# Kernel optimization log

Hardware: AMD Instinct MI355X
Metric: run time of the kernel (lower is better)

## Reference

```python
import jax, jax.numpy as jnp
import numpy as np
import math

NEG = -1000000.0


def setup_inputs() -> dict:
    key = jax.random.key(0)
    ks = jax.random.split(key, 8)
    B, S, D = 4, 2048, 1024
    std = 1.0 / math.sqrt(D)
    return {
        "queries": jax.random.normal(ks[0], (B, S, D), jnp.float32),
        "keys": jax.random.normal(ks[1], (B, S, D), jnp.float32),
        "values": jax.random.normal(ks[2], (B, S, D), jnp.float32),
        "valid_len": jax.random.randint(ks[3], (B,), 1, S, dtype=jnp.int64 if jax.config.jax_enable_x64 else jnp.int32),
        "W_q": jax.random.normal(ks[4], (D, D), jnp.float32) * std,
        "W_k": jax.random.normal(ks[5], (D, D), jnp.float32) * std,
        "W_v": jax.random.normal(ks[6], (D, D), jnp.float32) * std,
        "W_o": jax.random.normal(ks[7], (D, D), jnp.float32) * std,
    }


def reference(queries, keys, values, valid_len, W_q, W_k, W_v, W_o):
    NUM_HEADS = 16
    B, S, D = queries.shape
    hd = D // NUM_HEADS

    def split_heads(x):
        # (B, S, D) -> (B, H, S, hd)
        return x.reshape(B, -1, NUM_HEADS, hd).transpose(0, 2, 1, 3)

    # nn.Linear with weight W applies x @ W.T
    q = split_heads(queries @ W_q.T)
    k = split_heads(keys @ W_k.T)
    v = split_heads(values @ W_v.T)

    scale = 1.0 / math.sqrt(hd)
    scores = jnp.einsum('bhqd,bhkd->bhqk', q, k) * scale  # (B, H, Sq, Sk)

    # key-padding mask from valid_len: positions >= valid_len are masked
    kpos = jnp.arange(scores.shape[-1])
    pad_mask = kpos[None, None, None, :] >= valid_len[:, None, None, None]
    scores = jnp.where(pad_mask, NEG, scores)
    attn = jax.nn.softmax(scores, axis=-1)

    out = jnp.einsum('bhqk,bhkd->bhqd', attn, v)  # (B, H, Sq, hd)
    out = out.transpose(0, 2, 1, 3).reshape(B, -1, D)
    return out @ W_o.T
```

## Files before the change

kernel.cpp:

```cpp
#include <hip/hip_runtime.h>
#include <hip/hip_bf16.h>

using bf16_t = __bf16;
using bf16x8 = __attribute__((ext_vector_type(8))) __bf16;
using bf16x4 = __attribute__((ext_vector_type(4))) __bf16;
using bf16x2 = __attribute__((ext_vector_type(2))) __bf16;
using f32x4  = __attribute__((ext_vector_type(4))) float;

#define S_  2048
#define D_  1024

typedef __attribute__((address_space(1))) unsigned int glb_u32;
typedef __attribute__((address_space(3))) unsigned int lds_u32;

__device__ __forceinline__ void async_cp16(const void* g, void* lds) {
    __builtin_amdgcn_global_load_lds(
        (glb_u32*)(unsigned long long)g,
        (lds_u32*)(unsigned int)(unsigned long long)lds,
        16, 0, 0);
}

__global__ __launch_bounds__(256) void cast_f32_bf16(const float* __restrict__ s,
                                                     bf16_t* __restrict__ d, int n4) {
    int i = blockIdx.x * 256 + threadIdx.x;
    if (i >= n4) return;
    float4 f = reinterpret_cast<const float4*>(s)[i];
    bf16x4 o;
    o[0] = (bf16_t)f.x; o[1] = (bf16_t)f.y; o[2] = (bf16_t)f.z; o[3] = (bf16_t)f.w;
    reinterpret_cast<bf16x4*>(d)[i] = o;
}

__global__ __launch_bounds__(256) void cast2_f32_bf16(const float* __restrict__ a, const float* __restrict__ b,
                                                      bf16_t* __restrict__ oa, bf16_t* __restrict__ ob, int n4) {
    int i = blockIdx.x * 256 + threadIdx.x;
    if (i >= n4) return;
    const float* s = blockIdx.y ? b : a;
    bf16_t*      d = blockIdx.y ? ob : oa;
    float4 f = reinterpret_cast<const float4*>(s)[i];
    bf16x4 o;
    o[0] = (bf16_t)f.x; o[1] = (bf16_t)f.y; o[2] = (bf16_t)f.z; o[3] = (bf16_t)f.w;
    reinterpret_cast<bf16x4*>(d)[i] = o;
}

__global__ __launch_bounds__(256) void cast4_f32_bf16(const float* __restrict__ a, const float* __restrict__ b,
                                                      const float* __restrict__ c, const float* __restrict__ dd,
                                                      bf16_t* __restrict__ oa, bf16_t* __restrict__ ob,
                                                      bf16_t* __restrict__ oc, bf16_t* __restrict__ od, int n4) {
    int i = blockIdx.x * 256 + threadIdx.x;
    if (i >= n4) return;
    const float* s; bf16_t* d;
    int w = blockIdx.y;
    if      (w == 0) { s = a;  d = oa; }
    else if (w == 1) { s = b;  d = ob; }
    else if (w == 2) { s = c;  d = oc; }
    else             { s = dd; d = od; }
    float4 f = reinterpret_cast<const float4*>(s)[i];
    bf16x4 o;
    o[0] = (bf16_t)f.x; o[1] = (bf16_t)f.y; o[2] = (bf16_t)f.z; o[3] = (bf16_t)f.w;
    reinterpret_cast<bf16x4*>(d)[i] = o;
}

template <int OUTMODE>
__global__ __launch_bounds__(256) void gemm_bt(const bf16_t* __restrict__ A,
                                               const bf16_t* __restrict__ Bt,
                                               void* __restrict__ Cv, float scale) {
    __shared__ bf16_t As[2][128 * 32];
    __shared__ bf16_t Bs[2][128 * 32];
    const int K = 1024;
    int tid  = threadIdx.x;
    int lane = tid & 63;
    int w    = tid >> 6;
    int l15  = lane & 15, quad = lane >> 4;

    int bid = blockIdx.y * gridDim.x + blockIdx.x;
    int xcd = bid & 7, idx = bid >> 3;
    int m0 = (xcd * 8 + (idx & 7)) * 128;
    int n0 = (idx >> 3) * 128;
    int wm = (w >> 1) * 64, wn = (w & 1) * 64;

    const bf16_t* Ag = A  + (size_t)(m0 + (tid >> 2)) * K + (tid & 3) * 8;
    const bf16_t* Bg = Bt + (size_t)(n0 + (tid >> 2)) * K + (tid & 3) * 8;

    f32x4 acc[4][4] = {};

    async_cp16(Ag,                  &As[0][tid * 8]);
    async_cp16(Ag + (size_t)64 * K, &As[0][tid * 8 + 2048]);
    async_cp16(Bg,                  &Bs[0][tid * 8]);
    async_cp16(Bg + (size_t)64 * K, &Bs[0][tid * 8 + 2048]);
    __syncthreads();

    for (int k0 = 0; k0 < K; k0 += 32) {
        int cur = (k0 >> 5) & 1;
        if (k0 + 32 < K) {
            int nxt = cur ^ 1;
            async_cp16(Ag + k0 + 32,                  &As[nxt][tid * 8]);
            async_cp16(Ag + k0 + 32 + (size_t)64 * K, &As[nxt][tid * 8 + 2048]);
            async_cp16(Bg + k0 + 32,                  &Bs[nxt][tid * 8]);
            async_cp16(Bg + k0 + 32 + (size_t)64 * K, &Bs[nxt][tid * 8 + 2048]);
        }
        bf16x8 af[4], bfr[4];
#pragma unroll
        for (int t = 0; t < 4; t++) {
            af[t]  = *reinterpret_cast<const bf16x8*>(&As[cur][(wm + t * 16 + l15) * 32 + quad * 8]);
            bfr[t] = *reinterpret_cast<const bf16x8*>(&Bs[cur][(wn + t * 16 + l15) * 32 + quad * 8]);
        }
#pragma unroll
        for (int mt = 0; mt < 4; mt++)
#pragma unroll
            for (int nt = 0; nt < 4; nt++)
                acc[mt][nt] = __builtin_amdgcn_mfma_f32_16x16x32_bf16(af[mt], bfr[nt], acc[mt][nt], 0, 0, 0);
        __syncthreads();
    }

#pragma unroll
    for (int mt = 0; mt < 4; mt++)
#pragma unroll
        for (int nt = 0; nt < 4; nt++) {
            if (OUTMODE == 2) {
                int m = m0 + wm + mt * 16 + quad * 4;
                int n = n0 + wn + nt * 16 + l15;
                bf16x4 o4;
#pragma unroll
                for (int r = 0; r < 4; r++) o4[r] = (bf16_t)(acc[mt][nt][r] * scale);
                size_t vrow = (size_t)((m >> 11) * 16 + (n >> 6)) * 64 + (n & 63);
                int ml = m & 2047;
                int mp = (ml & ~31) | (((ml >> 2) & 3) << 3) | (((ml >> 4) & 1) << 2);
                *reinterpret_cast<bf16x4*>(&((bf16_t*)Cv)[vrow * S_ + mp]) = o4;
            } else {
#pragma unroll
                for (int r = 0; r < 4; r++) {
                    int m = m0 + wm + mt * 16 + quad * 4 + r;
                    int n = n0 + wn + nt * 16 + l15;
                    size_t idx2 = (size_t)m * 1024 + n;
                    if (OUTMODE == 1) reinterpret_cast<float*>(Cv)[idx2] = acc[mt][nt][r] * scale;
                    else              reinterpret_cast<bf16_t*>(Cv)[idx2] = (bf16_t)(acc[mt][nt][r] * scale);
                }
            }
        }
}

__global__ __launch_bounds__(256) void attn_fused(const bf16_t* __restrict__ Qp,
                                                  const bf16_t* __restrict__ Kp,
                                                  const bf16_t* __restrict__ Vt,
                                                  const int* __restrict__ vlen_p,
                                                  bf16_t* __restrict__ Out) {
    __shared__ bf16_t smem[4][64 * 64];

    int tid  = threadIdx.x;
    int lane = tid & 63, w = tid >> 6;
    int l15  = lane & 15, quad = lane >> 4;

    int nk[4], ord[4] = {0, 1, 2, 3};
#pragma unroll
    for (int i = 0; i < 4; i++) nk[i] = (vlen_p[i] + 63) >> 6;
#pragma unroll
    for (int i = 0; i < 3; i++)
#pragma unroll
        for (int j = 0; j < 3 - i; j++)
            if (nk[ord[j + 1]] > nk[ord[j]]) { int t = ord[j]; ord[j] = ord[j + 1]; ord[j + 1] = t; }

    int bid  = blockIdx.x;
    int b    = ord[bid >> 9];
    int t    = bid & 511;
    int h    = (t & 7) * 2 + ((t >> 3) & 1);
    int qblk = t >> 4;
    int vlen = vlen_p[b];
    int nkb  = (vlen + 63) >> 6;

    const bf16_t* Qg = Qp + (size_t)(b * S_ + qblk * 64) * D_ + h * 64;
    const bf16_t* Kg = Kp + (size_t)b * S_ * D_ + h * 64;
    const bf16_t* Vg = Vt + (size_t)(b * 16 + h) * 64 * S_;

    int r0 = tid >> 3, s0 = tid & 7;
    int sx = (s0 ^ (r0 & 7)) * 8;
    const bf16_t* kS0 = Kg + (size_t)r0 * D_ + sx;
    const bf16_t* kS1 = kS0 + (size_t)32 * D_;
    const bf16_t* vS0 = Vg + (size_t)r0 * S_ + sx;
    const bf16_t* vS1 = vS0 + (size_t)32 * S_;

    {
        const bf16_t* qS0 = Qg + (size_t)r0 * D_ + sx;
        async_cp16(qS0,                   smem[2] + tid * 8);
        async_cp16(qS0 + (size_t)32 * D_, smem[2] + tid * 8 + 2048);
        async_cp16(kS0, smem[0] + tid * 8);
        async_cp16(kS1, smem[0] + tid * 8 + 2048);
        async_cp16(vS0, smem[1] + tid * 8);
        async_cp16(vS1, smem[1] + tid * 8 + 2048);
    }
    __syncthreads();

    bf16x8 qf[2];
    {
        int row = w * 16 + l15, x = row & 7;
#pragma unroll
        for (int kk = 0; kk < 2; kk++)
            qf[kk] = *reinterpret_cast<const bf16x8*>(&smem[2][row * 64 + ((kk * 4 + quad) ^ x) * 8]);
    }
    __syncthreads();

    f32x4 o[4] = {};
    float l_st = 0.f;

    for (int kb = 0; kb < nkb; kb++) {
        int cur = kb & 1;
        if (kb + 1 < nkb) {
            int nxt = cur ^ 1;
            kS0 += (size_t)64 * D_; kS1 += (size_t)64 * D_;
            vS0 += 64;              vS1 += 64;
            async_cp16(kS0, smem[nxt * 2]     + tid * 8);
            async_cp16(kS1, smem[nxt * 2]     + tid * 8 + 2048);
            async_cp16(vS0, smem[nxt * 2 + 1] + tid * 8);
            async_cp16(vS1, smem[nxt * 2 + 1] + tid * 8 + 2048);
        }
        const bf16_t* Kc = smem[cur * 2];
        const bf16_t* Vc = smem[cur * 2 + 1];

        f32x4 sc[4] = {};
#pragma unroll
        for (int nt = 0; nt < 4; nt++) {
            int row = nt * 16 + l15, x = row & 7;
#pragma unroll
            for (int kk = 0; kk < 2; kk++) {
                bf16x8 kf = *reinterpret_cast<const bf16x8*>(&Kc[row * 64 + ((kk * 4 + quad) ^ x) * 8]);
                sc[nt] = __builtin_amdgcn_mfma_f32_16x16x32_bf16(kf, qf[kk], sc[nt], 0, 0, 0);
            }
        }

        bool partial = (vlen & 63) && (kb == nkb - 1);
        bf16x8 pf[2];
        float lacc = 0.f;
        if (!partial) {
#pragma unroll
            for (int nt = 0; nt < 4; nt++)
#pragma unroll
                for (int r = 0; r < 4; r++) {
                    float p = __builtin_exp2f(sc[nt][r]);
                    lacc += p;
                    pf[nt >> 1][(nt & 1) * 4 + r] = (bf16_t)p;
                }
        } else {
#pragma unroll
            for (int nt = 0; nt < 4; nt++)
#pragma unroll
                for (int r = 0; r < 4; r++) {
                    float p = __builtin_exp2f(sc[nt][r]);
                    if (kb * 64 + nt * 16 + quad * 4 + r >= vlen) p = 0.f;
                    lacc += p;
                    pf[nt >> 1][(nt & 1) * 4 + r] = (bf16_t)p;
                }
        }
        l_st += lacc;

#pragma unroll
        for (int np = 0; np < 2; np++)
#pragma unroll
            for (int dt = 0; dt < 4; dt++) {
                int row = dt * 16 + l15, x = row & 7;
                bf16x8 vf = *reinterpret_cast<const bf16x8*>(&Vc[row * 64 + ((np * 4 + quad) ^ x) * 8]);
                o[dt] = __builtin_amdgcn_mfma_f32_16x16x32_bf16(vf, pf[np], o[dt], 0, 0, 0);
            }

        __syncthreads();
    }

    float l = l_st;
    l += __shfl_xor(l, 16);
    l += __shfl_xor(l, 32);
    float inv = 1.0f / l;

    bf16_t* T = smem[0];
    {
        int row = w * 16 + l15, x = row & 7;
#pragma unroll
        for (int dt = 0; dt < 4; dt++) {
            bf16x4 o4;
#pragma unroll
            for (int r = 0; r < 4; r++) o4[r] = (bf16_t)(o[dt][r] * inv);
            int slot = dt * 2 + (quad >> 1);
            *reinterpret_cast<bf16x4*>(&T[row * 64 + (slot ^ x) * 8 + (quad & 1) * 4]) = o4;
        }
    }
    __syncthreads();
    {
        int row = tid >> 2, ch = tid & 3, x = row & 7;
        size_t obase = (size_t)(b * S_ + qblk * 64 + row) * D_ + h * 64 + ch * 16;
        bf16x8 f0 = *reinterpret_cast<const bf16x8*>(&T[row * 64 + ((ch * 2)     ^ x) * 8]);
        bf16x8 f1 = *reinterpret_cast<const bf16x8*>(&T[row * 64 + ((ch * 2 + 1) ^ x) * 8]);
        *reinterpret_cast<bf16x8*>(&Out[obase])     = f0;
        *reinterpret_cast<bf16x8*>(&Out[obase + 8]) = f1;
    }
}

extern "C" void kernel_launch(void* const* d_in, const int* in_sizes, int n_in,
                              void* d_out, int out_size, void* d_ws, size_t ws_size,
                              hipStream_t stream) {
    const float* q  = (const float*)d_in[0];
    const float* k  = (const float*)d_in[1];
    const float* v  = (const float*)d_in[2];
    const int*   vl = (const int*)d_in[3];
    const float* Wq = (const float*)d_in[4];
    const float* Wk = (const float*)d_in[5];
    const float* Wv = (const float*)d_in[6];
    const float* Wo = (const float*)d_in[7];
    float* out = (float*)d_out;

    bf16_t* ws = (bf16_t*)d_ws;
    const size_t SD = (size_t)8192 * 1024;
    const size_t WW = (size_t)1024 * 1024;
    bf16_t* tmpA = ws;
    bf16_t* tmpB = ws + SD;
    bf16_t* Qp   = ws + 2 * SD;
    bf16_t* Kp   = ws + 3 * SD;
    bf16_t* Vt   = ws + 4 * SD;
    bf16_t* Wqb  = ws + 5 * SD;
    bf16_t* Wkb  = Wqb + WW;
    bf16_t* Wvb  = Wqb + 2 * WW;
    bf16_t* Wob  = Wqb + 3 * WW;

    const float cs = 0.18033688f;
    dim3 blk(256);
    dim3 gg(8, 64);

    cast4_f32_bf16<<<dim3(1024, 4), blk, 0, stream>>>(Wq, Wk, Wv, Wo, Wqb, Wkb, Wvb, Wob, 262144);
    cast2_f32_bf16<<<dim3(8192, 2), blk, 0, stream>>>(q, k, tmpA, tmpB, 2097152);

    gemm_bt<0><<<gg, blk, 0, stream>>>(tmpA, Wqb, Qp, cs);
    gemm_bt<0><<<gg, blk, 0, stream>>>(tmpB, Wkb, Kp, 1.0f);
    cast_f32_bf16<<<dim3(8192), blk, 0, stream>>>(v, tmpA, 2097152);
    gemm_bt<2><<<gg, blk, 0, stream>>>(tmpA, Wvb, Vt, 1.0f);

    attn_fused<<<dim3(2048), blk, 0, stream>>>(Qp, Kp, Vt, vl, tmpB);
    gemm_bt<1><<<gg, blk, 0, stream>>>(tmpB, Wob, out, 1.0f);
}
```

Measured before the change: 322.9 us.

## Fuse fp32-to-bf16 activation casts into a single batched QKV GEMM kernel

Removes the separate cast kernels for queries, keys and values. The new QKV GEMM loads fp32 activations directly into registers, converts them to bf16 and stores them to LDS, which avoids writing and rereading the bf16 intermediates. The three projection GEMMs are merged into one launch with 1536 blocks, a z index selecting Q, K or V, to cut launch overhead and tail effects. The cost is that the A operand now goes through register-staged loads instead of async LDS copies and reads twice the bytes per element (fp32), which may add latency and register pressure.

```diff
diff --git a/kernel.cpp b/kernel.cpp
--- a/kernel.cpp
+++ b/kernel.cpp
@@ -18,28 +18,6 @@
         (glb_u32*)(unsigned long long)g,
         (lds_u32*)(unsigned int)(unsigned long long)lds,
         16, 0, 0);
-}
-
-__global__ __launch_bounds__(256) void cast_f32_bf16(const float* __restrict__ s,
-                                                     bf16_t* __restrict__ d, int n4) {
-    int i = blockIdx.x * 256 + threadIdx.x;
-    if (i >= n4) return;
-    float4 f = reinterpret_cast<const float4*>(s)[i];
-    bf16x4 o;
-    o[0] = (bf16_t)f.x; o[1] = (bf16_t)f.y; o[2] = (bf16_t)f.z; o[3] = (bf16_t)f.w;
-    reinterpret_cast<bf16x4*>(d)[i] = o;
-}
-
-__global__ __launch_bounds__(256) void cast2_f32_bf16(const float* __restrict__ a, const float* __restrict__ b,
-                                                      bf16_t* __restrict__ oa, bf16_t* __restrict__ ob, int n4) {
-    int i = blockIdx.x * 256 + threadIdx.x;
-    if (i >= n4) return;
-    const float* s = blockIdx.y ? b : a;
-    bf16_t*      d = blockIdx.y ? ob : oa;
-    float4 f = reinterpret_cast<const float4*>(s)[i];
-    bf16x4 o;
-    o[0] = (bf16_t)f.x; o[1] = (bf16_t)f.y; o[2] = (bf16_t)f.z; o[3] = (bf16_t)f.w;
-    reinterpret_cast<bf16x4*>(d)[i] = o;
 }
 
 __global__ __launch_bounds__(256) void cast4_f32_bf16(const float* __restrict__ a, const float* __restrict__ b,
@@ -60,10 +38,16 @@
     reinterpret_cast<bf16x4*>(d)[i] = o;
 }
 
-template <int OUTMODE>
-__global__ __launch_bounds__(256) void gemm_bt(const bf16_t* __restrict__ A,
-                                               const bf16_t* __restrict__ Bt,
-                                               void* __restrict__ Cv, float scale) {
+__global__ __launch_bounds__(256) void qkv_gemm(const float* __restrict__ qf,
+                                                const float* __restrict__ kf,
+                                                const float* __restrict__ vf,
+                                                const bf16_t* __restrict__ Wqb,
+                                                const bf16_t* __restrict__ Wkb,
+                                                const bf16_t* __restrict__ Wvb,
+                                                bf16_t* __restrict__ Qp,
+                                                bf16_t* __restrict__ Kp,
+                                                bf16_t* __restrict__ Vt,
+                                                float cs) {
     __shared__ bf16_t As[2][128 * 32];
     __shared__ bf16_t Bs[2][128 * 32];
     const int K = 1024;
@@ -72,7 +56,115 @@
     int w    = tid >> 6;
     int l15  = lane & 15, quad = lane >> 4;
 
-    int bid = blockIdx.y * gridDim.x + blockIdx.x;
+    int bid = blockIdx.x;
+    int xcd = bid & 7, idx = bid >> 3;
+    int z   = idx >> 6;
+    int rem = idx & 63;
+    int m0 = (xcd * 8 + (rem & 7)) * 128;
+    int n0 = (rem >> 3) * 128;
+    int wm = (w >> 1) * 64, wn = (w & 1) * 64;
+
+    const float*  Af; const bf16_t* Bt;
+    if      (z == 0) { Af = qf; Bt = Wqb; }
+    else if (z == 1) { Af = kf; Bt = Wkb; }
+    else             { Af = vf; Bt = Wvb; }
+    float scale = (z == 0) ? cs : 1.0f;
+
+    const float*  Ag = Af + (size_t)(m0 + (tid >> 2)) * K + (tid & 3) * 8;
+    const bf16_t* Bg = Bt + (size_t)(n0 + (tid >> 2)) * K + (tid & 3) * 8;
+
+    float4 a0, a1, a2, a3;
+    auto loadA = [&](int k0) {
+        const float* p = Ag + k0;
+        a0 = *reinterpret_cast<const float4*>(p);
+        a1 = *reinterpret_cast<const float4*>(p + 4);
+        a2 = *reinterpret_cast<const float4*>(p + (size_t)64 * K);
+        a3 = *reinterpret_cast<const float4*>(p + (size_t)64 * K + 4);
+    };
+    auto storeA = [&](bf16_t* dst) {
+        bf16x8 o0, o1;
+        o0[0] = (bf16_t)a0.x; o0[1] = (bf16_t)a0.y; o0[2] = (bf16_t)a0.z; o0[3] = (bf16_t)a0.w;
+        o0[4] = (bf16_t)a1.x; o0[5] = (bf16_t)a1.y; o0[6] = (bf16_t)a1.z; o0[7] = (bf16_t)a1.w;
+        o1[0] = (bf16_t)a2.x; o1[1] = (bf16_t)a2.y; o1[2] = (bf16_t)a2.z; o1[3] = (bf16_t)a2.w;
+        o1[4] = (bf16_t)a3.x; o1[5] = (bf16_t)a3.y; o1[6] = (bf16_t)a3.z; o1[7] = (bf16_t)a3.w;
+        *reinterpret_cast<bf16x8*>(dst + tid * 8)        = o0;
+        *reinterpret_cast<bf16x8*>(dst + tid * 8 + 2048) = o1;
+    };
+
+    f32x4 acc[4][4] = {};
+
+    loadA(0);
+    async_cp16(Bg,                  &Bs[0][tid * 8]);
+    async_cp16(Bg + (size_t)64 * K, &Bs[0][tid * 8 + 2048]);
+    storeA(As[0]);
+    __syncthreads();
+
+    for (int k0 = 0; k0 < K; k0 += 32) {
+        int cur = (k0 >> 5) & 1;
+        bool more = (k0 + 32 < K);
+        if (more) {
+            int nxt = cur ^ 1;
+            loadA(k0 + 32);
+            async_cp16(Bg + k0 + 32,                  &Bs[nxt][tid * 8]);
+            async_cp16(Bg + k0 + 32 + (size_t)64 * K, &Bs[nxt][tid * 8 + 2048]);
+        }
+        bf16x8 af[4], bfr[4];
+#pragma unroll
+        for (int t = 0; t < 4; t++) {
+            af[t]  = *reinterpret_cast<const bf16x8*>(&As[cur][(wm + t * 16 + l15) * 32 + quad * 8]);
+            bfr[t] = *reinterpret_cast<const bf16x8*>(&Bs[cur][(wn + t * 16 + l15) * 32 + quad * 8]);
+        }
+#pragma unroll
+        for (int mt = 0; mt < 4; mt++)
+#pragma unroll
+            for (int nt = 0; nt < 4; nt++)
+                acc[mt][nt] = __builtin_amdgcn_mfma_f32_16x16x32_bf16(af[mt], bfr[nt], acc[mt][nt], 0, 0, 0);
+        if (more) storeA(As[cur ^ 1]);
+        __syncthreads();
+    }
+
+    if (z == 2) {
+#pragma unroll
+        for (int mt = 0; mt < 4; mt++)
+#pragma unroll
+            for (int nt = 0; nt < 4; nt++) {
+                int m = m0 + wm + mt * 16 + quad * 4;
+                int n = n0 + wn + nt * 16 + l15;
+                bf16x4 o4;
+#pragma unroll
+                for (int r = 0; r < 4; r++) o4[r] = (bf16_t)acc[mt][nt][r];
+                size_t vrow = (size_t)((m >> 11) * 16 + (n >> 6)) * 64 + (n & 63);
+                int ml = m & 2047;
+                int mp = (ml & ~31) | (((ml >> 2) & 3) << 3) | (((ml >> 4) & 1) << 2);
+                *reinterpret_cast<bf16x4*>(&Vt[vrow * S_ + mp]) = o4;
+            }
+    } else {
+        bf16_t* Co = (z == 0) ? Qp : Kp;
+#pragma unroll
+        for (int mt = 0; mt < 4; mt++)
+#pragma unroll
+            for (int nt = 0; nt < 4; nt++)
+#pragma unroll
+                for (int r = 0; r < 4; r++) {
+                    int m = m0 + wm + mt * 16 + quad * 4 + r;
+                    int n = n0 + wn + nt * 16 + l15;
+                    Co[(size_t)m * 1024 + n] = (bf16_t)(acc[mt][nt][r] * scale);
+                }
+    }
+}
+
+__global__ __launch_bounds__(256) void gemm_out(const bf16_t* __restrict__ A,
+                                                const bf16_t* __restrict__ Bt,
+                                                float* __restrict__ C) {
+    __shared__ bf16_t As[2][128 * 32];
+    __shared__ bf16_t Bs[2][128 * 32];
+    const int K = 1024;
+    int tid  = threadIdx.x;
+    int lane = tid & 63;
+    int w    = tid >> 6;
+    int l15  = lane & 15, quad = lane >> 4;
+
+    int bid = blockIdx.x;
     int xcd = bid & 7, idx = bid >> 3;
     int m0 = (xcd * 8 + (idx & 7)) * 128;
     int n0 = (idx >> 3) * 128;
@@ -115,28 +207,13 @@
 #pragma unroll
     for (int mt = 0; mt < 4; mt++)
 #pragma unroll
-        for (int nt = 0; nt < 4; nt++) {
-            if (OUTMODE == 2) {
-                int m = m0 + wm + mt * 16 + quad * 4;
+        for (int nt = 0; nt < 4; nt++)
+#pragma unroll
+            for (int r = 0; r < 4; r++) {
+                int m = m0 + wm + mt * 16 + quad * 4 + r;
                 int n = n0 + wn + nt * 16 + l15;
-                bf16x4 o4;
-#pragma unroll
-                for (int r = 0; r < 4; r++) o4[r] = (bf16_t)(acc[mt][nt][r] * scale);
-                size_t vrow = (size_t)((m >> 11) * 16 + (n >> 6)) * 64 + (n & 63);
-                int ml = m & 2047;
-                int mp = (ml & ~31) | (((ml >> 2) & 3) << 3) | (((ml >> 4) & 1) << 2);
-                *reinterpret_cast<bf16x4*>(&((bf16_t*)Cv)[vrow * S_ + mp]) = o4;
-            } else {
-#pragma unroll
-                for (int r = 0; r < 4; r++) {
-                    int m = m0 + wm + mt * 16 + quad * 4 + r;
-                    int n = n0 + wn + nt * 16 + l15;
-                    size_t idx2 = (size_t)m * 1024 + n;
-                    if (OUTMODE == 1) reinterpret_cast<float*>(Cv)[idx2] = acc[mt][nt][r] * scale;
-                    else              reinterpret_cast<bf16_t*>(Cv)[idx2] = (bf16_t)(acc[mt][nt][r] * scale);
-                }
+                C[(size_t)m * 1024 + n] = acc[mt][nt][r];
             }
-        }
 }
 
 __global__ __launch_bounds__(256) void attn_fused(const bf16_t* __restrict__ Qp,
@@ -256,8 +333,8 @@
 #pragma unroll
             for (int dt = 0; dt < 4; dt++) {
                 int row = dt * 16 + l15, x = row & 7;
-                bf16x8 vf = *reinterpret_cast<const bf16x8*>(&Vc[row * 64 + ((np * 4 + quad) ^ x) * 8]);
-                o[dt] = __builtin_amdgcn_mfma_f32_16x16x32_bf16(vf, pf[np], o[dt], 0, 0, 0);
+                bf16x8 vfr = *reinterpret_cast<const bf16x8*>(&Vc[row * 64 + ((np * 4 + quad) ^ x) * 8]);
+                o[dt] = __builtin_amdgcn_mfma_f32_16x16x32_bf16(vfr, pf[np], o[dt], 0, 0, 0);
             }
 
         __syncthreads();
@@ -307,7 +384,6 @@
     bf16_t* ws = (bf16_t*)d_ws;
     const size_t SD = (size_t)8192 * 1024;
     const size_t WW = (size_t)1024 * 1024;
-    bf16_t* tmpA = ws;
     bf16_t* tmpB = ws + SD;
     bf16_t* Qp   = ws + 2 * SD;
     bf16_t* Kp   = ws + 3 * SD;
@@ -319,16 +395,9 @@
 
     const float cs = 0.18033688f;
     dim3 blk(256);
-    dim3 gg(8, 64);
 
     cast4_f32_bf16<<<dim3(1024, 4), blk, 0, stream>>>(Wq, Wk, Wv, Wo, Wqb, Wkb, Wvb, Wob, 262144);
-    cast2_f32_bf16<<<dim3(8192, 2), blk, 0, stream>>>(q, k, tmpA, tmpB, 2097152);
-
-    gemm_bt<0><<<gg, blk, 0, stream>>>(tmpA, Wqb, Qp, cs);
-    gemm_bt<0><<<gg, blk, 0, stream>>>(tmpB, Wkb, Kp, 1.0f);
-    cast_f32_bf16<<<dim3(8192), blk, 0, stream>>>(v, tmpA, 2097152);
-    gemm_bt<2><<<gg, blk, 0, stream>>>(tmpA, Wvb, Vt, 1.0f);
-
+    qkv_gemm<<<dim3(1536), blk, 0, stream>>>(q, k, v, Wqb, Wkb, Wvb, Qp, Kp, Vt, cs);
     attn_fused<<<dim3(2048), blk, 0, stream>>>(Qp, Kp, Vt, vl, tmpB);
-    gemm_bt<1><<<gg, blk, 0, stream>>>(tmpB, Wob, out, 1.0f);
-}
+    gemm_out<<<dim3(512), blk, 0, stream>>>(tmpB, Wob, out);
+}
```

After: 322.1 us. Within noise of the previous version (-0.3%).

## Fuse input casts into QKV GEMM with triple-buffered ring pipeline

Applied to the files above, without the earlier changes.

The separate fp32-to-bf16 cast kernels for queries, keys and values are removed. The projection GEMM now loads the fp32 activations directly into LDS and converts them to bf16 in registers. The three Q/K/V projections become a single 1536-block launch, and the GEMM moves from a double buffer with two syncs per step to a three-stage ring with explicit vmcnt waits, one barrier per step and XOR-swizzled LDS. This removes the bf16 intermediate round-trips and several launches, at the cost of doubled LDS for the fp32 A tiles and extra conversion work inside the main loop.

```diff
diff --git a/kernel.cpp b/kernel.cpp
--- a/kernel.cpp
+++ b/kernel.cpp
@@ -18,28 +18,6 @@
         (glb_u32*)(unsigned long long)g,
         (lds_u32*)(unsigned int)(unsigned long long)lds,
         16, 0, 0);
-}
-
-__global__ __launch_bounds__(256) void cast_f32_bf16(const float* __restrict__ s,
-                                                     bf16_t* __restrict__ d, int n4) {
-    int i = blockIdx.x * 256 + threadIdx.x;
-    if (i >= n4) return;
-    float4 f = reinterpret_cast<const float4*>(s)[i];
-    bf16x4 o;
-    o[0] = (bf16_t)f.x; o[1] = (bf16_t)f.y; o[2] = (bf16_t)f.z; o[3] = (bf16_t)f.w;
-    reinterpret_cast<bf16x4*>(d)[i] = o;
-}
-
-__global__ __launch_bounds__(256) void cast2_f32_bf16(const float* __restrict__ a, const float* __restrict__ b,
-                                                      bf16_t* __restrict__ oa, bf16_t* __restrict__ ob, int n4) {
-    int i = blockIdx.x * 256 + threadIdx.x;
-    if (i >= n4) return;
-    const float* s = blockIdx.y ? b : a;
-    bf16_t*      d = blockIdx.y ? ob : oa;
-    float4 f = reinterpret_cast<const float4*>(s)[i];
-    bf16x4 o;
-    o[0] = (bf16_t)f.x; o[1] = (bf16_t)f.y; o[2] = (bf16_t)f.z; o[3] = (bf16_t)f.w;
-    reinterpret_cast<bf16x4*>(d)[i] = o;
 }
 
 __global__ __launch_bounds__(256) void cast4_f32_bf16(const float* __restrict__ a, const float* __restrict__ b,
@@ -60,83 +38,177 @@
     reinterpret_cast<bf16x4*>(d)[i] = o;
 }
 
-template <int OUTMODE>
-__global__ __launch_bounds__(256) void gemm_bt(const bf16_t* __restrict__ A,
-                                               const bf16_t* __restrict__ Bt,
-                                               void* __restrict__ Cv, float scale) {
-    __shared__ bf16_t As[2][128 * 32];
-    __shared__ bf16_t Bs[2][128 * 32];
+template <int MODE>
+__global__ __launch_bounds__(256) void gemm_ring(const float* __restrict__ qf,
+                                                 const float* __restrict__ kf,
+                                                 const float* __restrict__ vf,
+                                                 const bf16_t* __restrict__ Wq,
+                                                 const bf16_t* __restrict__ Wk,
+                                                 const bf16_t* __restrict__ Wv,
+                                                 bf16_t* __restrict__ Qp,
+                                                 bf16_t* __restrict__ Kp,
+                                                 bf16_t* __restrict__ Vt,
+                                                 float cs,
+                                                 const bf16_t* __restrict__ Ab,
+                                                 const bf16_t* __restrict__ Wo,
+                                                 float* __restrict__ Co) {
+    constexpr int AE = (MODE == 0) ? 2 : 1;
+    __shared__ bf16_t As[3 * 128 * 32 * AE];
+    __shared__ bf16_t Bs[3 * 128 * 32];
     const int K = 1024;
     int tid  = threadIdx.x;
     int lane = tid & 63;
     int w    = tid >> 6;
     int l15  = lane & 15, quad = lane >> 4;
-
-    int bid = blockIdx.y * gridDim.x + blockIdx.x;
-    int xcd = bid & 7, idx = bid >> 3;
-    int m0 = (xcd * 8 + (idx & 7)) * 128;
-    int n0 = (idx >> 3) * 128;
     int wm = (w >> 1) * 64, wn = (w & 1) * 64;
 
-    const bf16_t* Ag = A  + (size_t)(m0 + (tid >> 2)) * K + (tid & 3) * 8;
-    const bf16_t* Bg = Bt + (size_t)(n0 + (tid >> 2)) * K + (tid & 3) * 8;
+    int bid = blockIdx.x;
+    int xcd = bid & 7, rem = bid >> 3;
+    int z = 0, r2 = rem;
+    if (MODE == 0) { z = rem >> 6; r2 = rem & 63; }
+    int m0 = (xcd * 8 + (r2 & 7)) * 128;
+    int n0 = (r2 >> 3) * 128;
+
+    const float*  Af = nullptr; const bf16_t* Ab16 = nullptr; const bf16_t* Bt;
+    if (MODE == 0) {
+        if      (z == 0) { Af = qf; Bt = Wq; }
+        else if (z == 1) { Af = kf; Bt = Wk; }
+        else             { Af = vf; Bt = Wv; }
+    } else { Ab16 = Ab; Bt = Wo; }
+
+    const float*  aSrcF[4]; bf16_t* aDstF[4];
+    const bf16_t* aSrcH[2]; bf16_t* aDstH[2];
+    const bf16_t* bSrc[2];  bf16_t* bDst[2];
+    if (MODE == 0) {
+#pragma unroll
+        for (int j = 0; j < 4; j++) {
+            int linear = j * 256 + tid;
+            int row = linear >> 3, s = linear & 7;
+            aSrcF[j] = Af + (size_t)(m0 + row) * K + (s ^ (row & 7)) * 4;
+            aDstF[j] = As + linear * 8;
+        }
+    } else {
+#pragma unroll
+        for (int j = 0; j < 2; j++) {
+            int linear = j * 256 + tid;
+            int row = linear >> 2, s = linear & 3;
+            aSrcH[j] = Ab16 + (size_t)(m0 + row) * K + (s ^ (row & 3)) * 8;
+            aDstH[j] = As + linear * 8;
+        }
+    }
+#pragma unroll
+    for (int j = 0; j < 2; j++) {
+        int linear = j * 256 + tid;
+        int row = linear >> 2, s = linear & 3;
+        bSrc[j] = Bt + (size_t)(n0 + row) * K + (s ^ (row & 3)) * 8;
+        bDst[j] = Bs + linear * 8;
+    }
+
+    constexpr int ASTG = (MODE == 0) ? 8192 : 4096;
+    auto stage = [&](int buf, int koff) {
+        if (MODE == 0) {
+#pragma unroll
+            for (int j = 0; j < 4; j++) async_cp16(aSrcF[j] + koff, aDstF[j] + buf * ASTG);
+        } else {
+#pragma unroll
+            for (int j = 0; j < 2; j++) async_cp16(aSrcH[j] + koff, aDstH[j] + buf * ASTG);
+        }
+#pragma unroll
+        for (int j = 0; j < 2; j++) async_cp16(bSrc[j] + koff, bDst[j] + buf * 4096);
+    };
 
     f32x4 acc[4][4] = {};
 
-    async_cp16(Ag,                  &As[0][tid * 8]);
-    async_cp16(Ag + (size_t)64 * K, &As[0][tid * 8 + 2048]);
-    async_cp16(Bg,                  &Bs[0][tid * 8]);
-    async_cp16(Bg + (size_t)64 * K, &Bs[0][tid * 8 + 2048]);
-    __syncthreads();
-
-    for (int k0 = 0; k0 < K; k0 += 32) {
-        int cur = (k0 >> 5) & 1;
-        if (k0 + 32 < K) {
-            int nxt = cur ^ 1;
-            async_cp16(Ag + k0 + 32,                  &As[nxt][tid * 8]);
-            async_cp16(Ag + k0 + 32 + (size_t)64 * K, &As[nxt][tid * 8 + 2048]);
-            async_cp16(Bg + k0 + 32,                  &Bs[nxt][tid * 8]);
-            async_cp16(Bg + k0 + 32 + (size_t)64 * K, &Bs[nxt][tid * 8 + 2048]);
-        }
+    stage(0, 0);
+    stage(1, 32);
+
+    int cur = 0, nx2 = 2;
+    for (int i = 0; i < 32; ++i) {
+        if (i == 31) {
+            asm volatile("s_waitcnt vmcnt(0)" ::: "memory");
+        } else if (MODE == 0) {
+            asm volatile("s_waitcnt vmcnt(6)" ::: "memory");
+        } else {
+            asm volatile("s_waitcnt vmcnt(4)" ::: "memory");
+        }
+        __builtin_amdgcn_s_barrier();
+        if (i + 2 < 32) stage(nx2, (i + 2) * 32);
+
         bf16x8 af[4], bfr[4];
-#pragma unroll
-        for (int t = 0; t < 4; t++) {
-            af[t]  = *reinterpret_cast<const bf16x8*>(&As[cur][(wm + t * 16 + l15) * 32 + quad * 8]);
-            bfr[t] = *reinterpret_cast<const bf16x8*>(&Bs[cur][(wn + t * 16 + l15) * 32 + quad * 8]);
+        if (MODE == 0) {
+            const float* AsF = reinterpret_cast<const float*>(As) + cur * 4096;
+#pragma unroll
+            for (int mt = 0; mt < 4; mt++) {
+                int row = wm + mt * 16 + l15, r7 = row & 7;
+                f32x4 v0 = *reinterpret_cast<const f32x4*>(&AsF[row * 32 + ((2 * quad)     ^ r7) * 4]);
+                f32x4 v1 = *reinterpret_cast<const f32x4*>(&AsF[row * 32 + ((2 * quad + 1) ^ r7) * 4]);
+#pragma unroll
+                for (int j = 0; j < 4; j++) { af[mt][j] = (bf16_t)v0[j]; af[mt][4 + j] = (bf16_t)v1[j]; }
+            }
+        } else {
+            const bf16_t* AsH = As + cur * 4096;
+#pragma unroll
+            for (int mt = 0; mt < 4; mt++) {
+                int row = wm + mt * 16 + l15;
+                af[mt] = *reinterpret_cast<const bf16x8*>(&AsH[row * 32 + (quad ^ (row & 3)) * 8]);
+            }
+        }
+        const bf16_t* Bsb = Bs + cur * 4096;
+#pragma unroll
+        for (int nt = 0; nt < 4; nt++) {
+            int row = wn + nt * 16 + l15;
+            bfr[nt] = *reinterpret_cast<const bf16x8*>(&Bsb[row * 32 + (quad ^ (row & 3)) * 8]);
         }
 #pragma unroll
         for (int mt = 0; mt < 4; mt++)
 #pragma unroll
             for (int nt = 0; nt < 4; nt++)
                 acc[mt][nt] = __builtin_amdgcn_mfma_f32_16x16x32_bf16(af[mt], bfr[nt], acc[mt][nt], 0, 0, 0);
-        __syncthreads();
-    }
-
-#pragma unroll
-    for (int mt = 0; mt < 4; mt++)
-#pragma unroll
-        for (int nt = 0; nt < 4; nt++) {
-            if (OUTMODE == 2) {
+
+        cur = (cur == 2) ? 0 : cur + 1;
+        nx2 = (nx2 == 2) ? 0 : nx2 + 1;
+    }
+
+    if (MODE == 0 && z == 2) {
+#pragma unroll
+        for (int mt = 0; mt < 4; mt++)
+#pragma unroll
+            for (int nt = 0; nt < 4; nt++) {
                 int m = m0 + wm + mt * 16 + quad * 4;
                 int n = n0 + wn + nt * 16 + l15;
                 bf16x4 o4;
 #pragma unroll
-                for (int r = 0; r < 4; r++) o4[r] = (bf16_t)(acc[mt][nt][r] * scale);
+                for (int r = 0; r < 4; r++) o4[r] = (bf16_t)acc[mt][nt][r];
                 size_t vrow = (size_t)((m >> 11) * 16 + (n >> 6)) * 64 + (n & 63);
                 int ml = m & 2047;
                 int mp = (ml & ~31) | (((ml >> 2) & 3) << 3) | (((ml >> 4) & 1) << 2);
-                *reinterpret_cast<bf16x4*>(&((bf16_t*)Cv)[vrow * S_ + mp]) = o4;
-            } else {
+                *reinterpret_cast<bf16x4*>(&Vt[vrow * S_ + mp]) = o4;
+            }
+    } else if (MODE == 0) {
+        bf16_t* CoH  = (z == 0) ? Qp : Kp;
+        float   scale = (z == 0) ? cs : 1.0f;
+#pragma unroll
+        for (int mt = 0; mt < 4; mt++)
+#pragma unroll
+            for (int nt = 0; nt < 4; nt++)
 #pragma unroll
                 for (int r = 0; r < 4; r++) {
                     int m = m0 + wm + mt * 16 + quad * 4 + r;
                     int n = n0 + wn + nt * 16 + l15;
-                    size_t idx2 = (size_t)m * 1024 + n;
-                    if (OUTMODE == 1) reinterpret_cast<float*>(Cv)[idx2] = acc[mt][nt][r] * scale;
-                    else              reinterpret_cast<bf16_t*>(Cv)[idx2] = (bf16_t)(acc[mt][nt][r] * scale);
+                    CoH[(size_t)m * 1024 + n] = (bf16_t)(acc[mt][nt][r] * scale);
                 }
-            }
-        }
+    } else {
+#pragma unroll
+        for (int mt = 0; mt < 4; mt++)
+#pragma unroll
+            for (int nt = 0; nt < 4; nt++)
+#pragma unroll
+                for (int r = 0; r < 4; r++) {
+                    int m = m0 + wm + mt * 16 + quad * 4 + r;
+                    int n = n0 + wn + nt * 16 + l15;
+                    Co[(size_t)m * 1024 + n] = acc[mt][nt][r];
+                }
+    }
 }
 
 __global__ __launch_bounds__(256) void attn_fused(const bf16_t* __restrict__ Qp,
@@ -256,8 +328,8 @@
 #pragma unroll
             for (int dt = 0; dt < 4; dt++) {
                 int row = dt * 16 + l15, x = row & 7;
-                bf16x8 vf = *reinterpret_cast<const bf16x8*>(&Vc[row * 64 + ((np * 4 + quad) ^ x) * 8]);
-                o[dt] = __builtin_amdgcn_mfma_f32_16x16x32_bf16(vf, pf[np], o[dt], 0, 0, 0);
+                bf16x8 vfr = *reinterpret_cast<const bf16x8*>(&Vc[row * 64 + ((np * 4 + quad) ^ x) * 8]);
+                o[dt] = __builtin_amdgcn_mfma_f32_16x16x32_bf16(vfr, pf[np], o[dt], 0, 0, 0);
             }
 
         __syncthreads();
@@ -307,7 +379,6 @@
     bf16_t* ws = (bf16_t*)d_ws;
     const size_t SD = (size_t)8192 * 1024;
     const size_t WW = (size_t)1024 * 1024;
-    bf16_t* tmpA = ws;
     bf16_t* tmpB = ws + SD;
     bf16_t* Qp   = ws + 2 * SD;
     bf16_t* Kp   = ws + 3 * SD;
@@ -319,16 +390,11 @@
 
     const float cs = 0.18033688f;
     dim3 blk(256);
-    dim3 gg(8, 64);
 
     cast4_f32_bf16<<<dim3(1024, 4), blk, 0, stream>>>(Wq, Wk, Wv, Wo, Wqb, Wkb, Wvb, Wob, 262144);
-    cast2_f32_bf16<<<dim3(8192, 2), blk, 0, stream>>>(q, k, tmpA, tmpB, 2097152);
-
-    gemm_bt<0><<<gg, blk, 0, stream>>>(tmpA, Wqb, Qp, cs);
-    gemm_bt<0><<<gg, blk, 0, stream>>>(tmpB, Wkb, Kp, 1.0f);
-    cast_f32_bf16<<<dim3(8192), blk, 0, stream>>>(v, tmpA, 2097152);
-    gemm_bt<2><<<gg, blk, 0, stream>>>(tmpA, Wvb, Vt, 1.0f);
-
+    gemm_ring<0><<<dim3(1536), blk, 0, stream>>>(q, k, v, Wqb, Wkb, Wvb, Qp, Kp, Vt, cs,
+                                                 nullptr, nullptr, nullptr);
     attn_fused<<<dim3(2048), blk, 0, stream>>>(Qp, Kp, Vt, vl, tmpB);
-    gemm_bt<1><<<gg, blk, 0, stream>>>(tmpB, Wob, out, 1.0f);
+    gemm_ring<1><<<dim3(512), blk, 0, stream>>>(nullptr, nullptr, nullptr, nullptr, nullptr, nullptr,
+                                                nullptr, nullptr, nullptr, 1.0f, tmpB, Wob, out);
 }
```

Result: slower. 334.1 us (+3.4%).
